# Kernel tuning notes

Measured on AMD Instinct MI355X. Metric: run time of the kernel, lower is better.

The kernel has to match this reference:

```python
import jax, jax.numpy as jnp
import numpy as np

EMBED_DIM = 1024
N_HEADS = 16
D_HEAD = EMBED_DIM // N_HEADS


def setup_inputs() -> dict:
    key = jax.random.key(0)
    kx, kq, kk, kv = jax.random.split(key, 4)
    x = jax.random.normal(kx, (2, 2048, EMBED_DIM), dtype=jnp.float32)
    Wq = jax.random.normal(kq, (EMBED_DIM, EMBED_DIM), dtype=jnp.float32) * 0.02
    Wk = jax.random.normal(kk, (EMBED_DIM, EMBED_DIM), dtype=jnp.float32) * 0.02
    Wv = jax.random.normal(kv, (EMBED_DIM, EMBED_DIM), dtype=jnp.float32) * 0.02
    return {"x": x, "Wq": Wq, "Wk": Wk, "Wv": Wv}


def reference(x, Wq, Wk, Wv):
    B, N, D = x.shape
    H, Dh = N_HEADS, D_HEAD
    # Fused QKV projections, then split heads: [B, N, D] -> [B, H, N, Dh]
    q = (x @ Wq).reshape(B, N, H, Dh).transpose(0, 2, 1, 3)
    k = (x @ Wk).reshape(B, N, H, Dh).transpose(0, 2, 1, 3)
    v = (x @ Wv).reshape(B, N, H, Dh).transpose(0, 2, 1, 3)
    scale = 1.0 / jnp.sqrt(jnp.asarray(Dh, dtype=x.dtype))
    scores = jnp.einsum("bhqd,bhkd->bhqk", q, k) * scale  # [B, H, N, N]
    attn = jax.nn.softmax(scores, axis=-1)
    out = jnp.einsum("bhqk,bhkd->bhqd", attn, v)  # [B, H, N, Dh]
    return out.transpose(0, 2, 1, 3).reshape(B, N, D)
```

## Files before the change

### kernel.cpp

```cpp
#include <hip/hip_runtime.h>
#include <cstdint>

typedef __bf16 bf16;
typedef __bf16 bf16x4 __attribute__((ext_vector_type(4)));
typedef __bf16 bf16x8 __attribute__((ext_vector_type(8)));
typedef float floatx4 __attribute__((ext_vector_type(4)));
typedef float f32x16 __attribute__((ext_vector_type(16)));
typedef unsigned int uint2v __attribute__((ext_vector_type(2)));
typedef unsigned int uint4v __attribute__((ext_vector_type(4)));

typedef const __attribute__((address_space(1))) void* as1_cvptr;
typedef __attribute__((address_space(3))) void* as3_vptr;

__device__ __forceinline__ void gl_lds16(const void* g, void* l) {
  __builtin_amdgcn_global_load_lds((as1_cvptr)(uintptr_t)g,
                                   (as3_vptr)(uint32_t)(uintptr_t)l, 16, 0, 0);
}

#define EMBED 1024
#define SEQ 2048
#define NH 16
#define DH 64
#define QSCALE 0.18033688f

__device__ __forceinline__ unsigned pk_bf16(float a, float b) {
  unsigned short ua = __builtin_bit_cast(unsigned short, (bf16)a);
  unsigned short ub = __builtin_bit_cast(unsigned short, (bf16)b);
  return (unsigned)ua | ((unsigned)ub << 16);
}

__global__ __launch_bounds__(256) void prep(
    const float* __restrict__ x, const float* __restrict__ Wq,
    const float* __restrict__ Wk, const float* __restrict__ Wv,
    bf16* __restrict__ xb, bf16* __restrict__ Wqt,
    bf16* __restrict__ Wkt, bf16* __restrict__ Wvt) {
  __shared__ __align__(16) bf16 tile[64][72];
  int z = blockIdx.y;
  int t = threadIdx.x;
  if (z == 3) {
    size_t base = ((size_t)blockIdx.x * 256 + t) * 8;
#pragma unroll
    for (int it = 0; it < 8; ++it) {
      size_t i = base + (size_t)it * (256 * 256 * 8);
      floatx4 a = *(const floatx4*)(x + i);
      floatx4 bv = *(const floatx4*)(x + i + 4);
      bf16x8 o;
#pragma unroll
      for (int j = 0; j < 4; ++j) { o[j] = (bf16)a[j]; o[4 + j] = (bf16)bv[j]; }
      *(bf16x8*)(xb + i) = o;
    }
    return;
  }
  const float* W = (z == 0) ? Wq : (z == 1) ? Wk : Wv;
  bf16* Wt = (z == 0) ? Wqt : (z == 1) ? Wkt : Wvt;
  int k0 = (blockIdx.x >> 4) * 64, n0 = (blockIdx.x & 15) * 64;
  int r = t >> 3, c = (t & 7) * 8;
#pragma unroll
  for (int half = 0; half < 2; ++half) {
    const float* src = &W[(size_t)(k0 + r + half * 32) * EMBED + n0 + c];
    floatx4 f0 = *(const floatx4*)src;
    floatx4 f1 = *(const floatx4*)(src + 4);
    bf16x8 o;
#pragma unroll
    for (int j = 0; j < 4; ++j) { o[j] = (bf16)f0[j]; o[4 + j] = (bf16)f1[j]; }
    *(bf16x8*)&tile[r + half * 32][c] = o;
  }
  __syncthreads();
#pragma unroll
  for (int p = 0; p < 2; ++p) {
    int nn = (t >> 3) + p * 32, kk = (t & 7) * 8;
    bf16x8 v;
#pragma unroll
    for (int i = 0; i < 8; ++i) v[i] = tile[kk + i][nn];
    *(bf16x8*)&Wt[(size_t)(n0 + nn) * EMBED + k0 + kk] = v;
  }
}

__global__ __launch_bounds__(256) void qkv3(
    const bf16* __restrict__ Xb, const bf16* __restrict__ Wqt,
    const bf16* __restrict__ Wkt, const bf16* __restrict__ Wvt,
    bf16* __restrict__ qo, bf16* __restrict__ ko, bf16* __restrict__ vto) {
  __shared__ __align__(16) bf16 As[128 * 32];
  __shared__ __align__(16) bf16 Bs[128 * 32];

  int gid = blockIdx.x;
  int z = gid % 3;
  int rem = gid / 3;
  int bxx = rem & 7, byy = rem >> 3;

  const bf16* Wt = (z == 0) ? Wqt : (z == 1) ? Wkt : Wvt;
  bf16* out = (z == 0) ? qo : (z == 1) ? ko : vto;
  int m0 = (z == 2 ? bxx : byy) * 128;
  int n0 = (z == 2 ? byy : bxx) * 128;
  const bf16* Asrc = (z == 2) ? Wt : Xb;
  const bf16* Bsrc = (z == 2) ? Xb : Wt;
  float oscale = (z == 0) ? QSCALE : 1.0f;

  int t = threadIdx.x;
  int w = t >> 6, lane = t & 63, ln = lane & 15, quad = lane >> 4;
  int wm = (w >> 1) * 64, wn = (w & 1) * 64;

  floatx4 acc[4][4];
#pragma unroll
  for (int i = 0; i < 4; ++i)
#pragma unroll
    for (int j = 0; j < 4; ++j) acc[i][j] = floatx4{0.f, 0.f, 0.f, 0.f};

  int sr = t >> 2, sc = (t & 3) * 8;
  const bf16* ag = Asrc + (size_t)(m0 + sr) * EMBED + sc;
  const bf16* bg = Bsrc + (size_t)(n0 + sr) * EMBED + sc;
  bf16* al = As + sr * 32 + sc;
  bf16* bl = Bs + sr * 32 + sc;

  for (int k0 = 0; k0 < EMBED; k0 += 32) {
    __syncthreads();
    gl_lds16(ag + k0, al);
    gl_lds16(ag + k0 + (size_t)64 * EMBED, al + 64 * 32);
    gl_lds16(bg + k0, bl);
    gl_lds16(bg + k0 + (size_t)64 * EMBED, bl + 64 * 32);
    __syncthreads();

    bf16x8 afr[4], bfr[4];
#pragma unroll
    for (int i = 0; i < 4; ++i)
      afr[i] = *(const bf16x8*)&As[(wm + i * 16 + ln) * 32 + quad * 8];
#pragma unroll
    for (int j = 0; j < 4; ++j)
      bfr[j] = *(const bf16x8*)&Bs[(wn + j * 16 + ln) * 32 + quad * 8];
#pragma unroll
    for (int i = 0; i < 4; ++i)
#pragma unroll
      for (int j = 0; j < 4; ++j)
        acc[i][j] =
            __builtin_amdgcn_mfma_f32_16x16x32_bf16(afr[i], bfr[j], acc[i][j], 0, 0, 0);
  }

#pragma unroll
  for (int i = 0; i < 4; ++i) {
#pragma unroll
    for (int r = 0; r < 4; ++r) {
      int row = m0 + wm + i * 16 + quad * 4 + r;
#pragma unroll
      for (int j = 0; j < 4; ++j) {
        int col = n0 + wn + j * 16 + ln;
        float v = acc[i][j][r] * oscale;
        size_t dst;
        if (z != 2) {
          int b = row >> 11, ns = row & 2047, h = col >> 6, d = col & 63;
          dst = ((size_t)((b * NH + h) * SEQ + ns)) * DH + d;
        } else {
          int h = row >> 6, d = row & 63, b = col >> 11, ns = col & 2047;
          dst = ((size_t)((b * NH + h) * DH + d)) * SEQ + ns;
        }
        out[dst] = (bf16)v;
      }
    }
  }
}

__global__ __launch_bounds__(1024, 4) void flash(
    const bf16* __restrict__ Qg, const bf16* __restrict__ Kg,
    const bf16* __restrict__ Vtg, float* __restrict__ Og) {
  __shared__ __align__(16) char smem[147456];
  bf16* Ks = (bf16*)smem;
  bf16* Vs = (bf16*)(smem + 73728);
  float* Om = (float*)smem;
  float* Lm = (float*)(smem + 34816);

  int t = threadIdx.x;
  int lane = t & 63, w = t >> 6;
  int col = lane & 31, hi = lane >> 5;
  int qg = w >> 2, split = w & 3;
  int bh = blockIdx.y;
  int b = bh >> 4, h = bh & 15;
  const bf16* Q = Qg + (size_t)bh * SEQ * DH;
  const bf16* K = Kg + (size_t)bh * SEQ * DH;
  const bf16* Vt = Vtg + (size_t)bh * DH * SEQ;
  int q0 = blockIdx.x * 128 + qg * 32;

  bf16x8 bq[4];
#pragma unroll
  for (int kc = 0; kc < 4; ++kc)
    bq[kc] = *(const bf16x8*)&Q[(size_t)(q0 + col) * DH + kc * 16 + hi * 8];

  f32x16 oacc[2];
#pragma unroll
  for (int m = 0; m < 2; ++m)
#pragma unroll
    for (int r = 0; r < 16; ++r) oacc[m][r] = 0.f;
  float li = 0.f;

  int ss = t >> 8, st = t & 255;
  int kr = st >> 2, kcol = (st & 3) * 16;
  const bf16* kg = K + ((size_t)(ss * 512 + kr)) * DH + kcol;
  const bf16* vg = Vt + (size_t)kr * SEQ + ss * 512 + kcol;
  bf16* kl = Ks + ss * 4608 + kr * 72 + kcol;
  bf16* vl = Vs + ss * 4608 + kr * 72 + kcol;

  bf16x8 pk0 = *(const bf16x8*)kg;
  bf16x8 pk1 = *(const bf16x8*)(kg + 8);
  bf16x8 pv0 = *(const bf16x8*)vg;
  bf16x8 pv1 = *(const bf16x8*)(vg + 8);

  const bf16* Kb = Ks + split * 4608;
  const bf16* Vb = Vs + split * 4608;

  for (int it = 0; it < 8; ++it) {
    int buf = (it & 1) * 18432;
    *(bf16x8*)(kl + buf) = pk0;
    *(bf16x8*)(kl + buf + 8) = pk1;
    *(bf16x8*)(vl + buf) = pv0;
    *(bf16x8*)(vl + buf + 8) = pv1;
    __syncthreads();

    if (it + 1 < 8) {
      size_t ko = (size_t)(it + 1) * 64 * DH;
      pk0 = *(const bf16x8*)(kg + ko);
      pk1 = *(const bf16x8*)(kg + ko + 8);
      pv0 = *(const bf16x8*)(vg + (it + 1) * 64);
      pv1 = *(const bf16x8*)(vg + (it + 1) * 64 + 8);
    }
    const bf16* Kt = Kb + buf;
    const bf16* Vtb = Vb + buf;

#pragma unroll
    for (int mt = 0; mt < 2; ++mt) {
      f32x16 s;
#pragma unroll
      for (int r = 0; r < 16; ++r) s[r] = 0.f;
#pragma unroll
      for (int kc = 0; kc < 4; ++kc) {
        bf16x8 ak = *(const bf16x8*)&Kt[(mt * 32 + col) * 72 + kc * 16 + hi * 8];
        s = __builtin_amdgcn_mfma_f32_32x32x16_bf16(ak, bq[kc], s, 0, 0, 0);
      }
#pragma unroll
      for (int cc = 0; cc < 2; ++cc) {
        int rb = cc * 8;
        float e0 = exp2f(s[rb + 0]), e1 = exp2f(s[rb + 1]);
        float e2 = exp2f(s[rb + 2]), e3 = exp2f(s[rb + 3]);
        float e4 = exp2f(s[rb + 4]), e5 = exp2f(s[rb + 5]);
        float e6 = exp2f(s[rb + 6]), e7 = exp2f(s[rb + 7]);
        li += ((e0 + e1) + (e2 + e3)) + ((e4 + e5) + (e6 + e7));
        unsigned lo0 = pk_bf16(e0, e1), lo1 = pk_bf16(e2, e3);
        unsigned h0 = pk_bf16(e4, e5), h1 = pk_bf16(e6, e7);
        uint2v r02 = __builtin_amdgcn_permlane32_swap(lo0, h0, false, false);
        uint2v r13 = __builtin_amdgcn_permlane32_swap(lo1, h1, false, false);
        uint4v uu;
        uu[0] = r02[0]; uu[1] = r13[0]; uu[2] = r02[1]; uu[3] = r13[1];
        bf16x8 pb = __builtin_bit_cast(bf16x8, uu);

        int c = mt * 2 + cc;
        bf16x8 av0 = *(const bf16x8*)&Vtb[(col) * 72 + c * 16 + hi * 8];
        bf16x8 av1 = *(const bf16x8*)&Vtb[(32 + col) * 72 + c * 16 + hi * 8];
        oacc[0] = __builtin_amdgcn_mfma_f32_32x32x16_bf16(av0, pb, oacc[0], 0, 0, 0);
        oacc[1] = __builtin_amdgcn_mfma_f32_32x32x16_bf16(av1, pb, oacc[1], 0, 0, 0);
      }
    }
  }

  li += __shfl_xor(li, 32, 64);
  if (lane < 32) Lm[split * 128 + qg * 32 + col] = li;

#pragma unroll 1
  for (int rs = 1; rs < 4; ++rs) {
    if (split == rs) {
#pragma unroll
      for (int m = 0; m < 2; ++m)
#pragma unroll
        for (int rr = 0; rr < 4; ++rr) {
          floatx4 v4;
#pragma unroll
          for (int j = 0; j < 4; ++j) v4[j] = oacc[m][rr * 4 + j];
          *(floatx4*)&Om[(qg * 32 + col) * 68 + m * 32 + rr * 8 + hi * 4] = v4;
        }
    }
    __syncthreads();
    if (split == 0) {
#pragma unroll
      for (int m = 0; m < 2; ++m)
#pragma unroll
        for (int rr = 0; rr < 4; ++rr) {
          floatx4 v4 =
              *(const floatx4*)&Om[(qg * 32 + col) * 68 + m * 32 + rr * 8 + hi * 4];
#pragma unroll
          for (int j = 0; j < 4; ++j) oacc[m][rr * 4 + j] += v4[j];
        }
    }
    __syncthreads();
  }
  if (split == 0) {
#pragma unroll
    for (int m = 0; m < 2; ++m)
#pragma unroll
      for (int rr = 0; rr < 4; ++rr) {
        floatx4 v4;
#pragma unroll
        for (int j = 0; j < 4; ++j) v4[j] = oacc[m][rr * 4 + j];
        *(floatx4*)&Om[(qg * 32 + col) * 68 + m * 32 + rr * 8 + hi * 4] = v4;
      }
  }
  __syncthreads();

#pragma unroll
  for (int rep = 0; rep < 2; ++rep) {
    int idx = rep * 1024 + t;
    int q = idx >> 4, dc = (idx & 15) * 4;
    float lt = Lm[q] + Lm[128 + q] + Lm[256 + q] + Lm[384 + q];
    float inv = 1.0f / lt;
    floatx4 ov = *(const floatx4*)&Om[q * 68 + dc];
    ov[0] *= inv; ov[1] *= inv; ov[2] *= inv; ov[3] *= inv;
    int ns = blockIdx.x * 128 + q;
    *(floatx4*)&Og[((size_t)(b * SEQ + ns)) * EMBED + h * DH + dc] = ov;
  }
}

extern "C" void kernel_launch(void* const* d_in, const int* in_sizes, int n_in,
                              void* d_out, int out_size, void* d_ws, size_t ws_size,
                              hipStream_t stream) {
  const int XEL = 2 * 2048 * 1024;
  const float *x, *Wq, *Wk, *Wv;
  if (in_sizes[0] == XEL) {
    x = (const float*)d_in[0];
    Wq = (const float*)d_in[1];
    Wk = (const float*)d_in[2];
    Wv = (const float*)d_in[3];
  } else {
    Wk = (const float*)d_in[0];
    Wq = (const float*)d_in[1];
    Wv = (const float*)d_in[2];
    x = (const float*)d_in[3];
  }
  bf16* ws = (bf16*)d_ws;

  const size_t M1 = 1024 * 1024;
  bf16* q_ws = ws;
  bf16* k_ws = ws + 4 * M1;
  bf16* vt_ws = ws + 8 * M1;
  bf16* wqt = ws + 12 * M1;
  bf16* wkt = ws + 13 * M1;
  bf16* wvt = ws + 14 * M1;
  bf16* xb = ws + 15 * M1;

  prep<<<dim3(256, 4), 256, 0, stream>>>(x, Wq, Wk, Wv, xb, wqt, wkt, wvt);
  qkv3<<<dim3(768), 256, 0, stream>>>(xb, wqt, wkt, wvt, q_ws, k_ws, vt_ws);
  flash<<<dim3(16, 32), 1024, 0, stream>>>(q_ws, k_ws, vt_ws, (float*)d_out);
}
```

Baseline: 184.7 us.

## Restructure flash to 512 threads with direct-to-LDS swizzled loads, vectorize QKV stores

The flash kernel drops from 16 waves with a 4-way key split and a 144KB LDS buffer to 8 waves with a 2-way split and a 36KB LDS buffer. K and V^T tiles are now loaded with global_load_lds straight into an XOR-swizzled LDS layout over 16 iterations, replacing register-staged double buffering, and the cross-split reduction becomes a single pass. The QKV projection swaps operand roles so each lane writes four contiguous bf16 values per store instead of scalar scattered writes. The aim is more resident blocks, fewer LDS bank conflicts and fewer stores. The cost is that loads are no longer overlapped with compute, since each iteration syncs before and after its load.

```diff
diff --git a/kernel.cpp b/kernel.cpp
--- a/kernel.cpp
+++ b/kernel.cpp
@@ -90,10 +90,10 @@
 
   const bf16* Wt = (z == 0) ? Wqt : (z == 1) ? Wkt : Wvt;
   bf16* out = (z == 0) ? qo : (z == 1) ? ko : vto;
-  int m0 = (z == 2 ? bxx : byy) * 128;
-  int n0 = (z == 2 ? byy : bxx) * 128;
-  const bf16* Asrc = (z == 2) ? Wt : Xb;
-  const bf16* Bsrc = (z == 2) ? Xb : Wt;
+  int m0 = (z == 2 ? byy : bxx) * 128;
+  int n0 = (z == 2 ? bxx : byy) * 128;
+  const bf16* Asrc = (z == 2) ? Xb : Wt;
+  const bf16* Bsrc = (z == 2) ? Wt : Xb;
   float oscale = (z == 0) ? QSCALE : 1.0f;
 
   int t = threadIdx.x;
@@ -135,42 +135,51 @@
             __builtin_amdgcn_mfma_f32_16x16x32_bf16(afr[i], bfr[j], acc[i][j], 0, 0, 0);
   }
 
-#pragma unroll
-  for (int i = 0; i < 4; ++i) {
-#pragma unroll
-    for (int r = 0; r < 4; ++r) {
-      int row = m0 + wm + i * 16 + quad * 4 + r;
+  if (z != 2) {
+#pragma unroll
+    for (int i = 0; i < 4; ++i) {
+      int od = m0 + wm + i * 16 + quad * 4;
+      int hq = od >> 6, d0 = od & 63;
 #pragma unroll
       for (int j = 0; j < 4; ++j) {
-        int col = n0 + wn + j * 16 + ln;
-        float v = acc[i][j][r] * oscale;
-        size_t dst;
-        if (z != 2) {
-          int b = row >> 11, ns = row & 2047, h = col >> 6, d = col & 63;
-          dst = ((size_t)((b * NH + h) * SEQ + ns)) * DH + d;
-        } else {
-          int h = row >> 6, d = row & 63, b = col >> 11, ns = col & 2047;
-          dst = ((size_t)((b * NH + h) * DH + d)) * SEQ + ns;
-        }
-        out[dst] = (bf16)v;
-      }
-    }
-  }
-}
-
-__global__ __launch_bounds__(1024, 4) void flash(
+        int c = n0 + wn + j * 16 + ln;
+        int bb = c >> 11, ns = c & 2047;
+        bf16x4 pv;
+#pragma unroll
+        for (int r = 0; r < 4; ++r) pv[r] = (bf16)(acc[i][j][r] * oscale);
+        *(bf16x4*)&out[(((size_t)(bb * NH + hq)) * SEQ + ns) * DH + d0] = pv;
+      }
+    }
+  } else {
+#pragma unroll
+    for (int i = 0; i < 4; ++i) {
+      int sq = m0 + wm + i * 16 + quad * 4;
+      int bb = sq >> 11, ns0 = sq & 2047;
+#pragma unroll
+      for (int j = 0; j < 4; ++j) {
+        int od = n0 + wn + j * 16 + ln;
+        int hq = od >> 6, d = od & 63;
+        bf16x4 pv;
+#pragma unroll
+        for (int r = 0; r < 4; ++r) pv[r] = (bf16)acc[i][j][r];
+        *(bf16x4*)&out[(((size_t)(bb * NH + hq)) * DH + d) * SEQ + ns0] = pv;
+      }
+    }
+  }
+}
+
+__global__ __launch_bounds__(512, 6) void flash(
     const bf16* __restrict__ Qg, const bf16* __restrict__ Kg,
     const bf16* __restrict__ Vtg, float* __restrict__ Og) {
-  __shared__ __align__(16) char smem[147456];
-  bf16* Ks = (bf16*)smem;
-  bf16* Vs = (bf16*)(smem + 73728);
+  __shared__ __align__(16) char smem[36864];
+  char* sm = smem;
   float* Om = (float*)smem;
   float* Lm = (float*)(smem + 34816);
 
   int t = threadIdx.x;
   int lane = t & 63, w = t >> 6;
   int col = lane & 31, hi = lane >> 5;
-  int qg = w >> 2, split = w & 3;
+  int qg = w >> 1, split = w & 1;
   int bh = blockIdx.y;
   int b = bh >> 4, h = bh & 15;
   const bf16* Q = Qg + (size_t)bh * SEQ * DH;
@@ -190,38 +199,40 @@
     for (int r = 0; r < 16; ++r) oacc[m][r] = 0.f;
   float li = 0.f;
 
-  int ss = t >> 8, st = t & 255;
-  int kr = st >> 2, kcol = (st & 3) * 16;
-  const bf16* kg = K + ((size_t)(ss * 512 + kr)) * DH + kcol;
-  const bf16* vg = Vt + (size_t)kr * SEQ + ss * 512 + kcol;
-  bf16* kl = Ks + ss * 4608 + kr * 72 + kcol;
-  bf16* vl = Vs + ss * 4608 + kr * 72 + kcol;
-
-  bf16x8 pk0 = *(const bf16x8*)kg;
-  bf16x8 pk1 = *(const bf16x8*)(kg + 8);
-  bf16x8 pv0 = *(const bf16x8*)vg;
-  bf16x8 pv1 = *(const bf16x8*)(vg + 8);
-
-  const bf16* Kb = Ks + split * 4608;
-  const bf16* Vb = Vs + split * 4608;
-
-  for (int it = 0; it < 8; ++it) {
-    int buf = (it & 1) * 18432;
-    *(bf16x8*)(kl + buf) = pk0;
-    *(bf16x8*)(kl + buf + 8) = pk1;
-    *(bf16x8*)(vl + buf) = pv0;
-    *(bf16x8*)(vl + buf + 8) = pv1;
+  int xaddr[4];
+#pragma unroll
+  for (int k2 = 0; k2 < 4; ++k2)
+    xaddr[k2] = split * 8192 + col * 128 + ((((col & 7) ^ (k2 * 2 + hi))) << 4);
+
+  int rs = w >> 2, ra = (w >> 1) & 1, rh = w & 1;
+  int row0 = lane >> 3;
+  int cswz = (lane & 7) ^ (row0 & 7);
+  const char* gsrc;
+  int ldsb, itstride, istride;
+  if (ra == 0) {
+    gsrc = (const char*)K + ((size_t)rs * 1024 + rh * 32 + row0) * 128 + cswz * 16;
+    ldsb = rs * 8192 + rh * 4096;
+    itstride = 8192;
+    istride = 1024;
+  } else {
+    gsrc = (const char*)Vt + ((size_t)(rh * 32 + row0)) * 4096 + rs * 2048 + cswz * 16;
+    ldsb = 16384 + rs * 8192 + rh * 4096;
+    itstride = 128;
+    istride = 32768;
+  }
+
+#pragma unroll 1
+  for (int it = 0; it < 16; ++it) {
     __syncthreads();
-
-    if (it + 1 < 8) {
-      size_t ko = (size_t)(it + 1) * 64 * DH;
-      pk0 = *(const bf16x8*)(kg + ko);
-      pk1 = *(const bf16x8*)(kg + ko + 8);
-      pv0 = *(const bf16x8*)(vg + (it + 1) * 64);
-      pv1 = *(const bf16x8*)(vg + (it + 1) * 64 + 8);
-    }
-    const bf16* Kt = Kb + buf;
-    const bf16* Vtb = Vb + buf;
+    {
+      const char* gs = gsrc + (size_t)it * itstride;
+      char* ld = sm + ldsb + lane * 16;
+      gl_lds16(gs, ld);
+      gl_lds16(gs + istride, ld + 1024);
+      gl_lds16(gs + 2 * istride, ld + 2048);
+      gl_lds16(gs + 3 * istride, ld + 3072);
+    }
+    __syncthreads();
 
 #pragma unroll
     for (int mt = 0; mt < 2; ++mt) {
@@ -230,7 +241,7 @@
       for (int r = 0; r < 16; ++r) s[r] = 0.f;
 #pragma unroll
       for (int kc = 0; kc < 4; ++kc) {
-        bf16x8 ak = *(const bf16x8*)&Kt[(mt * 32 + col) * 72 + kc * 16 + hi * 8];
+        bf16x8 ak = *(const bf16x8*)(sm + xaddr[kc] + mt * 4096);
         s = __builtin_amdgcn_mfma_f32_32x32x16_bf16(ak, bq[kc], s, 0, 0, 0);
       }
 #pragma unroll
@@ -250,8 +261,8 @@
         bf16x8 pb = __builtin_bit_cast(bf16x8, uu);
 
         int c = mt * 2 + cc;
-        bf16x8 av0 = *(const bf16x8*)&Vtb[(col) * 72 + c * 16 + hi * 8];
-        bf16x8 av1 = *(const bf16x8*)&Vtb[(32 + col) * 72 + c * 16 + hi * 8];
+        bf16x8 av0 = *(const bf16x8*)(sm + xaddr[c] + 16384);
+        bf16x8 av1 = *(const bf16x8*)(sm + xaddr[c] + 16384 + 4096);
         oacc[0] = __builtin_amdgcn_mfma_f32_32x32x16_bf16(av0, pb, oacc[0], 0, 0, 0);
         oacc[1] = __builtin_amdgcn_mfma_f32_32x32x16_bf16(av1, pb, oacc[1], 0, 0, 0);
       }
@@ -259,36 +270,9 @@
   }
 
   li += __shfl_xor(li, 32, 64);
+  __syncthreads();
   if (lane < 32) Lm[split * 128 + qg * 32 + col] = li;
-
-#pragma unroll 1
-  for (int rs = 1; rs < 4; ++rs) {
-    if (split == rs) {
-#pragma unroll
-      for (int m = 0; m < 2; ++m)
-#pragma unroll
-        for (int rr = 0; rr < 4; ++rr) {
-          floatx4 v4;
-#pragma unroll
-          for (int j = 0; j < 4; ++j) v4[j] = oacc[m][rr * 4 + j];
-          *(floatx4*)&Om[(qg * 32 + col) * 68 + m * 32 + rr * 8 + hi * 4] = v4;
-        }
-    }
-    __syncthreads();
-    if (split == 0) {
-#pragma unroll
-      for (int m = 0; m < 2; ++m)
-#pragma unroll
-        for (int rr = 0; rr < 4; ++rr) {
-          floatx4 v4 =
-              *(const floatx4*)&Om[(qg * 32 + col) * 68 + m * 32 + rr * 8 + hi * 4];
-#pragma unroll
-          for (int j = 0; j < 4; ++j) oacc[m][rr * 4 + j] += v4[j];
-        }
-    }
-    __syncthreads();
-  }
-  if (split == 0) {
+  if (split == 1) {
 #pragma unroll
     for (int m = 0; m < 2; ++m)
 #pragma unroll
@@ -300,12 +284,25 @@
       }
   }
   __syncthreads();
-
-#pragma unroll
-  for (int rep = 0; rep < 2; ++rep) {
-    int idx = rep * 1024 + t;
+  if (split == 0) {
+#pragma unroll
+    for (int m = 0; m < 2; ++m)
+#pragma unroll
+      for (int rr = 0; rr < 4; ++rr) {
+        floatx4 v4 =
+            *(const floatx4*)&Om[(qg * 32 + col) * 68 + m * 32 + rr * 8 + hi * 4];
+#pragma unroll
+        for (int j = 0; j < 4; ++j) v4[j] += oacc[m][rr * 4 + j];
+        *(floatx4*)&Om[(qg * 32 + col) * 68 + m * 32 + rr * 8 + hi * 4] = v4;
+      }
+  }
+  __syncthreads();
+
+#pragma unroll
+  for (int rep = 0; rep < 4; ++rep) {
+    int idx = rep * 512 + t;
     int q = idx >> 4, dc = (idx & 15) * 4;
-    float lt = Lm[q] + Lm[128 + q] + Lm[256 + q] + Lm[384 + q];
+    float lt = Lm[q] + Lm[128 + q];
     float inv = 1.0f / lt;
     floatx4 ov = *(const floatx4*)&Om[q * 68 + dc];
     ov[0] *= inv; ov[1] *= inv; ov[2] *= inv; ov[3] *= inv;
@@ -343,5 +340,5 @@
 
   prep<<<dim3(256, 4), 256, 0, stream>>>(x, Wq, Wk, Wv, xb, wqt, wkt, wvt);
   qkv3<<<dim3(768), 256, 0, stream>>>(xb, wqt, wkt, wvt, q_ws, k_ws, vt_ws);
-  flash<<<dim3(16, 32), 1024, 0, stream>>>(q_ws, k_ws, vt_ws, (float*)d_out);
-}
+  flash<<<dim3(16, 32), 512, 0, stream>>>(q_ws, k_ws, vt_ws, (float*)d_out);
+}
```

Result: slower. 233.2 us (+26.3%).
